# Optimization experiments

Measured on AMD Instinct MI355X. Metric: run time of the kernel, lower is better.

The kernel has to match this reference:

```python
import math
import jax, jax.numpy as jnp
import numpy as np

HEADS = 8
LOG_APPROX_VAR = math.log(0.01)  # self.var = 0.01, non-trainable


def clustering(x, approx_log_var, mu, log_var, log_prior):
    """Faithful port of DisentangledAttention.clustering (mi_estimation=False).
    x: [B,H,L,D]; approx_log_var: [B,H,L]; mu/log_var: [H,C,D]; log_prior: [H,C].
    Returns (cluster_probs [B,H,L,C], kl_loss [B,1,1], div_loss [B])."""
    B, H, L, D = x.shape
    xe = x[:, :, :, None, :]                      # [B,H,L,1,D]
    mue = mu[:, None, :, :]                       # [H,1,C,D]
    alv = approx_log_var[:, :, :, None, None]     # [B,H,L,1,1]
    avar = jnp.exp(alv)
    lv = log_var[:, None, :, :]                   # [H,1,C,D]
    var = jnp.exp(lv)
    logp = jax.nn.log_softmax(log_prior, axis=-1)  # [H,C]

    mse = (xe - mue) ** 2 / var                   # [B,H,L,C,D]
    log_pdf = -0.5 * mse.sum(-1) - D * math.pi - 0.5 * lv.sum(-1)  # [B,H,L,C]
    log_pdf = log_pdf + logp[:, None, :]
    log_probs = jax.nn.log_softmax(log_pdf, axis=-1)
    probs = jnp.exp(log_probs)                    # [B,H,L,C]

    logp_b = logp[None, :, None, :]               # broadcast prior log-probs
    prior = jnp.exp(logp_b)
    # F.kl_div(log_probs, prior) = prior * (log(prior) - log_probs)
    kl = (prior * (logp_b - log_probs)).sum(-1).mean(axis=(1, 2))            # [B]
    kl = kl + 0.5 * (probs * (mse + avar / var + lv).sum(-1)).sum(-1).mean(axis=(1, 2))
    kl = kl - 0.5 * jnp.mean(((1.0 + alv).sum(-1)) * D, axis=(1, 2, 3))
    kl_loss = kl.reshape(-1, 1, 1)

    eyeL = jnp.eye(L, dtype=x.dtype)
    div = jnp.einsum('bhqc,bhkc->bhqk', probs, probs)   # [B,H,L,L]
    div = (div - eyeL) ** 2
    wmask = eyeL * 1.25 + (1.0 - eyeL) * 0.75
    div_loss = (div * wmask).mean(axis=(1, 2, 3))       # [B]
    return probs, kl_loss, div_loss


def setup_inputs() -> dict:
    k = jax.random.key(0)
    ks = jax.random.split(k, 10)
    B, L, D, H, C = 4, 1024, 512, HEADS, 8
    Dk = D // H
    lin_std = 1.0 / math.sqrt(2.0 * D)  # xavier_normal gain=1/sqrt(2)
    return {
        'query': jax.random.normal(ks[0], (B, L, D), jnp.float32),
        'key': jax.random.normal(ks[1], (B, L, D), jnp.float32),
        'value': jax.random.normal(ks[2], (B, L, D), jnp.float32),
        'padding_mask': jnp.zeros((B, 1, L), jnp.float32),
        'Wq': jax.random.normal(ks[3], (D, D), jnp.float32) * lin_std,
        'bq': jnp.zeros((D,), jnp.float32),
        'Wk': jax.random.normal(ks[4], (D, D), jnp.float32) * lin_std,
        'bk': jnp.zeros((D,), jnp.float32),
        'Wv': jax.random.normal(ks[5], (D, D), jnp.float32) * lin_std,
        'bv': jnp.zeros((D,), jnp.float32),
        'Wo': jax.random.normal(ks[6], (D, D), jnp.float32) * lin_std,
        'bo': jnp.zeros((D,), jnp.float32),
        'tok_mu': jax.random.normal(ks[7], (H, C, Dk), jnp.float32) * 0.1,
        'tok_log_var': jnp.zeros((H, C, Dk), jnp.float32),
        'tok_log_prior': jnp.full((H, C), math.log(1.0 / C), jnp.float32),
    }


def reference(query, key, value, padding_mask, Wq, bq, Wk, bk, Wv, bv, Wo, bo,
              tok_mu, tok_log_var, tok_log_prior):
    B, L, D = query.shape
    H = HEADS
    Dk = D // H

    # GMM clustering on raw (unprojected) per-head query/key, eval mode (no reparam noise)
    qh = query.reshape(B, L, H, Dk).transpose(0, 2, 1, 3)  # [B,H,L,Dk]
    kh = key.reshape(B, L, H, Dk).transpose(0, 2, 1, 3)
    alv = jnp.full((B, H, L), LOG_APPROX_VAR, dtype=query.dtype)
    probs_q, kl_q, div_q = clustering(qh, alv, tok_mu, tok_log_var, tok_log_prior)
    probs_k, kl_k, div_k = clustering(kh, alv, tok_mu, tok_log_var, tok_log_prior)

    # Disentangled mask: tokens sharing clusters attend (mask==1 means blocked)
    sim = jnp.einsum('bhqc,bhkc->bhqk', probs_q, probs_k)   # [B,H,L,L]
    cmask = jnp.clip(1.0 - sim + padding_mask[:, :, None, :], 0.0, 1.0)

    # Projections + scaled softmax attention (per softmax_attention/full_attention)
    q = (query @ Wq.T + bq).reshape(B, L, H, Dk).transpose(0, 2, 1, 3) / math.sqrt(Dk)
    kk = (key @ Wk.T + bk).reshape(B, L, H, Dk).transpose(0, 2, 1, 3)
    v = (value @ Wv.T + bv).reshape(B, L, H, Dk).transpose(0, 2, 1, 3)
    scores = jnp.einsum('bhqd,bhkd->bhqk', q, kk) + jax.lax.stop_gradient(cmask) * (-10000.0)
    attn = jax.nn.softmax(scores, axis=-1) * (1.0 - cmask)
    out = jnp.einsum('bhqk,bhkd->bhqd', attn, v).transpose(0, 2, 1, 3).reshape(B, L, D)
    out = out @ Wo.T + bo

    kl_loss = kl_q + kl_k                      # [B,1,1]
    div_loss = (div_q + div_k).reshape(-1, 1, 1)  # [B,1,1]
    return out, kl_loss, div_loss
```

## Files before the change

kernel.cpp:

```cpp
#include <hip/hip_runtime.h>
#include <hip/hip_bf16.h>
#include <math.h>

#define NB 4
#define NL 1024
#define ND 512
#define NH 8
#define NC 8
#define NDK 64

static constexpr float KL3_CONST = 115.36544595161891f;

typedef __bf16 bf16x8 __attribute__((ext_vector_type(8)));
typedef float  f32x4v __attribute__((ext_vector_type(4)));
typedef unsigned short u16x4 __attribute__((ext_vector_type(4)));
typedef unsigned short u16x8 __attribute__((ext_vector_type(8)));

__device__ __forceinline__ unsigned short bf16u(float f) {
    return __builtin_bit_cast(unsigned short, (__bf16)f);
}

struct GemmArgs {
    const void* A; const float* W; const float* bias; void* out;
    float scale; int abf; int obf; int brow; int ostr; int vmap;
};

#define GEMM_BUF 15360

__device__ __forceinline__ void gemm_body(const GemmArgs& g, unsigned char* smem)
{
    const int tid = threadIdx.x;
    int n0, m0;
    if (g.vmap) {
        const int linear = blockIdx.y * 4 + blockIdx.x;
        n0 = (linear & 31) * 128;
        m0 = (linear >> 5) * 64;
    } else {
        n0 = blockIdx.x * 128;
        m0 = blockIdx.y * 64;
    }

    const int w = tid >> 6, lane = tid & 63;
    const int r16 = lane & 15, quad = lane >> 4;
    const int arow = tid >> 2, akc = tid & 3;
    const int wrow = tid >> 1, wkc = tid & 1;

    f32x4v acc[8];
#pragma unroll
    for (int n = 0; n < 8; ++n) acc[n] = (f32x4v){0.f, 0.f, 0.f, 0.f};

    auto ldA = [&](int k0) -> u16x8 {
        if (g.abf) {
            return *(const u16x8*)((const unsigned short*)g.A + (size_t)(m0 + arow) * 512 + k0 + akc * 8);
        }
        const float* ap = (const float*)g.A + (size_t)(m0 + arow) * 512 + k0 + akc * 8;
        const float4 a0 = *(const float4*)ap, a1 = *(const float4*)(ap + 4);
        return (u16x8){ bf16u(a0.x), bf16u(a0.y), bf16u(a0.z), bf16u(a0.w),
                        bf16u(a1.x), bf16u(a1.y), bf16u(a1.z), bf16u(a1.w) };
    };
    auto ldW = [&](int k0, u16x8* dst) {
        const float* wp = (const float*)g.W + (size_t)(n0 + wrow) * 512 + k0 + wkc * 16;
        const float4 w0 = *(const float4*)wp,       w1 = *(const float4*)(wp + 4);
        const float4 w2 = *(const float4*)(wp + 8), w3 = *(const float4*)(wp + 12);
        dst[0] = (u16x8){ bf16u(w0.x), bf16u(w0.y), bf16u(w0.z), bf16u(w0.w),
                          bf16u(w1.x), bf16u(w1.y), bf16u(w1.z), bf16u(w1.w) };
        dst[1] = (u16x8){ bf16u(w2.x), bf16u(w2.y), bf16u(w2.z), bf16u(w2.w),
                          bf16u(w3.x), bf16u(w3.y), bf16u(w3.z), bf16u(w3.w) };
    };
    auto store_stage = [&](int buf, const u16x8& sa, const u16x8* sw) {
        unsigned short* As = (unsigned short*)(smem + buf * GEMM_BUF);
        unsigned short* Ws = (unsigned short*)(smem + buf * GEMM_BUF + 5120);
        *(u16x8*)(As + arow * 40 + akc * 8) = sa;
        *(u16x8*)(Ws + wrow * 40 + wkc * 16) = sw[0];
        *(u16x8*)(Ws + wrow * 40 + wkc * 16 + 8) = sw[1];
    };
    auto mfma_half = [&](int buf) {
        unsigned short* As = (unsigned short*)(smem + buf * GEMM_BUF);
        unsigned short* Ws = (unsigned short*)(smem + buf * GEMM_BUF + 5120);
        bf16x8 af = *(const bf16x8*)(As + (w * 16 + r16) * 40 + quad * 8);
#pragma unroll
        for (int ni = 0; ni < 8; ++ni) {
            bf16x8 bfr = *(const bf16x8*)(Ws + (ni * 16 + r16) * 40 + quad * 8);
            acc[ni] = __builtin_amdgcn_mfma_f32_16x16x32_bf16(af, bfr, acc[ni], 0, 0, 0);
        }
    };

    u16x8 sa0 = ldA(0),  sw0[2]; ldW(0, sw0);
    u16x8 sa1 = ldA(32), sw1[2]; ldW(32, sw1);
    store_stage(0, sa0, sw0);
    sa0 = ldA(64); ldW(64, sw0);

    for (int p = 0; p < 16; p += 2) {
        const int kbase = p * 32;
        __syncthreads();
        store_stage(1, sa1, sw1);
        if (kbase + 96 < 512) { sa1 = ldA(kbase + 96); ldW(kbase + 96, sw1); }
        mfma_half(0);

        __syncthreads();
        if (p + 2 < 16) store_stage(0, sa0, sw0);
        if (kbase + 128 < 512) { sa0 = ldA(kbase + 128); ldW(kbase + 128, sw0); }
        mfma_half(1);
    }

#pragma unroll
    for (int ni = 0; ni < 8; ++ni) {
        const int col = n0 + ni * 16 + r16;
        const float bcol = g.brow ? 0.f : g.bias[col];
#pragma unroll
        for (int i = 0; i < 4; ++i) {
            const int row = m0 + w * 16 + quad * 4 + i;
            const float bv = g.brow ? g.bias[row] : bcol;
            const float v = (acc[ni][i] + bv) * g.scale;
            if (g.obf) ((unsigned short*)g.out)[(size_t)row * g.ostr + col] = bf16u(v);
            else       ((float*)g.out)[(size_t)row * g.ostr + col] = v;
        }
    }
}

#define GEMM_BUF64 10240

__device__ __forceinline__ void gemm_body64(const GemmArgs& g, unsigned char* smem)
{
    const int tid = threadIdx.x;
    const int n0 = blockIdx.x * 64, m0 = blockIdx.y * 64;

    const int w = tid >> 6, lane = tid & 63;
    const int r16 = lane & 15, quad = lane >> 4;
    const int arow = tid >> 2, akc = tid & 3;

    f32x4v acc[4];
#pragma unroll
    for (int n = 0; n < 4; ++n) acc[n] = (f32x4v){0.f, 0.f, 0.f, 0.f};

    auto ldA = [&](int k0) -> u16x8 {
        if (g.abf) {
            return *(const u16x8*)((const unsigned short*)g.A + (size_t)(m0 + arow) * 512 + k0 + akc * 8);
        }
        const float* ap = (const float*)g.A + (size_t)(m0 + arow) * 512 + k0 + akc * 8;
        const float4 a0 = *(const float4*)ap, a1 = *(const float4*)(ap + 4);
        return (u16x8){ bf16u(a0.x), bf16u(a0.y), bf16u(a0.z), bf16u(a0.w),
                        bf16u(a1.x), bf16u(a1.y), bf16u(a1.z), bf16u(a1.w) };
    };
    auto ldW8 = [&](int k0) -> u16x8 {
        const float* wp = (const float*)g.W + (size_t)(n0 + arow) * 512 + k0 + akc * 8;
        const float4 w0 = *(const float4*)wp, w1 = *(const float4*)(wp + 4);
        return (u16x8){ bf16u(w0.x), bf16u(w0.y), bf16u(w0.z), bf16u(w0.w),
                        bf16u(w1.x), bf16u(w1.y), bf16u(w1.z), bf16u(w1.w) };
    };
    auto store_stage = [&](int buf, const u16x8& sa, const u16x8& sw) {
        unsigned short* As = (unsigned short*)(smem + buf * GEMM_BUF64);
        unsigned short* Ws = (unsigned short*)(smem + buf * GEMM_BUF64 + 5120);
        *(u16x8*)(As + arow * 40 + akc * 8) = sa;
        *(u16x8*)(Ws + arow * 40 + akc * 8) = sw;
    };
    auto mfma_half = [&](int buf) {
        unsigned short* As = (unsigned short*)(smem + buf * GEMM_BUF64);
        unsigned short* Ws = (unsigned short*)(smem + buf * GEMM_BUF64 + 5120);
        bf16x8 af = *(const bf16x8*)(As + (w * 16 + r16) * 40 + quad * 8);
#pragma unroll
        for (int ni = 0; ni < 4; ++ni) {
            bf16x8 bfr = *(const bf16x8*)(Ws + (ni * 16 + r16) * 40 + quad * 8);
            acc[ni] = __builtin_amdgcn_mfma_f32_16x16x32_bf16(af, bfr, acc[ni], 0, 0, 0);
        }
    };

    u16x8 sa0 = ldA(0),  sw0 = ldW8(0);
    u16x8 sa1 = ldA(32), sw1 = ldW8(32);
    store_stage(0, sa0, sw0);
    sa0 = ldA(64); sw0 = ldW8(64);

    for (int p = 0; p < 16; p += 2) {
        const int kbase = p * 32;
        __syncthreads();
        store_stage(1, sa1, sw1);
        if (kbase + 96 < 512) { sa1 = ldA(kbase + 96); sw1 = ldW8(kbase + 96); }
        mfma_half(0);

        __syncthreads();
        if (p + 2 < 16) store_stage(0, sa0, sw0);
        if (kbase + 128 < 512) { sa0 = ldA(kbase + 128); sw0 = ldW8(kbase + 128); }
        mfma_half(1);
    }

#pragma unroll
    for (int ni = 0; ni < 4; ++ni) {
        const int col = n0 + ni * 16 + r16;
        const float bcol = g.brow ? 0.f : g.bias[col];
#pragma unroll
        for (int i = 0; i < 4; ++i) {
            const int row = m0 + w * 16 + quad * 4 + i;
            const float bv = g.brow ? g.bias[row] : bcol;
            const float v = (acc[ni][i] + bv) * g.scale;
            if (g.obf) ((unsigned short*)g.out)[(size_t)row * g.ostr + col] = bf16u(v);
            else       ((float*)g.out)[(size_t)row * g.ostr + col] = v;
        }
    }
}

__device__ __forceinline__ void cluster_body(
    const float* __restrict__ query, const float* __restrict__ key,
    const float* __restrict__ tok_mu, const float* __restrict__ tok_log_var,
    const float* __restrict__ tok_log_prior,
    float* __restrict__ probs_q, float* __restrict__ probs_k,
    float* __restrict__ klp, float* __restrict__ divp, float* __restrict__ Gp,
    int linear, unsigned char* smem)
{
    float* mu_s    = (float*)smem;
    float* iv_s    = (float*)(smem + 2048);
    float* Pl      = (float*)(smem + 4096);
    float* Gpart   = (float*)(smem + 13312);
    float* red_s   = (float*)(smem + 14336);
    float* lvsum_s = (float*)(smem + 14368);
    float* alpha_s = (float*)(smem + 14400);
    float* logp_s  = (float*)(smem + 14432);
    float* prior_s = (float*)(smem + 14464);

    const int tid  = threadIdx.x;
    const int side = linear >> 7;
    const int rem  = linear & 127;
    const int bh   = rem >> 2, chunk = rem & 3;
    const int b    = bh >> 3, h = bh & 7;
    const int blocklin = side * 128 + bh * 4 + chunk;
    const float* src = side ? key : query;
    float* probs_out = side ? probs_k : probs_q;

    for (int i = tid; i < 512; i += 256) {
        mu_s[i] = tok_mu[h * 512 + i];
        float lv = tok_log_var[h * 512 + i];
        iv_s[i] = __expf(-lv);
    }
    if (tid < 8) {
        float ls = 0.f, al = 0.f;
        for (int d = 0; d < 64; ++d) {
            float lv = tok_log_var[(h * 8 + tid) * 64 + d];
            ls += lv;
            al += 0.01f * __expf(-lv) + lv;
        }
        lvsum_s[tid] = ls; alpha_s[tid] = al;
    }
    if (tid == 0) {
        float lp[8]; float mx = -1e30f;
        for (int c = 0; c < 8; ++c) { lp[c] = tok_log_prior[h * 8 + c]; mx = fmaxf(mx, lp[c]); }
        float se = 0.f;
        for (int c = 0; c < 8; ++c) se += __expf(lp[c] - mx);
        float lse = mx + __logf(se);
        for (int c = 0; c < 8; ++c) { logp_s[c] = lp[c] - lse; prior_s[c] = __expf(lp[c] - lse); }
    }
    __syncthreads();

    const int l = chunk * 256 + tid;
    const float4* xp = (const float4*)(src + ((size_t)(b * NL + l)) * ND + h * NDK);
    float4 xr[16];
#pragma unroll
    for (int i = 0; i < 16; ++i) xr[i] = xp[i];

    float ms[8];
#pragma unroll
    for (int c = 0; c < 8; ++c) {
        const float4* mc = (const float4*)(mu_s + c * 64);
        const float4* ic = (const float4*)(iv_s + c * 64);
        float s = 0.f;
#pragma unroll
        for (int i = 0; i < 16; ++i) {
            float4 m4 = mc[i], v4 = ic[i], x4 = xr[i];
            float dx = x4.x - m4.x; s = fmaf(dx * dx, v4.x, s);
            float dy = x4.y - m4.y; s = fmaf(dy * dy, v4.y, s);
            float dz = x4.z - m4.z; s = fmaf(dz * dz, v4.z, s);
            float dw = x4.w - m4.w; s = fmaf(dw * dw, v4.w, s);
        }
        ms[c] = s;
    }

    float lpdf[8]; float mx = -1e30f;
#pragma unroll
    for (int c = 0; c < 8; ++c) {
        lpdf[c] = -0.5f * (ms[c] + lvsum_s[c]) + logp_s[c];
        mx = fmaxf(mx, lpdf[c]);
    }
    float e[8]; float se = 0.f;
#pragma unroll
    for (int c = 0; c < 8; ++c) { e[c] = __expf(lpdf[c] - mx); se += e[c]; }
    float lse = __logf(se);
    float inv = 1.f / se;
    float p[8]; float kl1 = 0.f, kl2 = 0.f, sqq = 0.f;
#pragma unroll
    for (int c = 0; c < 8; ++c) {
        p[c] = e[c] * inv;
        float logprob = lpdf[c] - mx - lse;
        kl1 += prior_s[c] * (logp_s[c] - logprob);
        kl2 += p[c] * (ms[c] + alpha_s[c]);
        sqq = fmaf(p[c], p[c], sqq);
    }

    float* po = probs_out + ((size_t)((b * NH + h) * NL + l)) * NC;
    ((float4*)po)[0] = make_float4(p[0], p[1], p[2], p[3]);
    ((float4*)po)[1] = make_float4(p[4], p[5], p[6], p[7]);
#pragma unroll
    for (int c = 0; c < 8; ++c) Pl[tid * 9 + c] = p[c];

    float dterm = 1.25f * (sqq - 1.f) * (sqq - 1.f) - 0.75f * sqq * sqq;
    float klv = kl1 + 0.5f * kl2;
    __syncthreads();

    {
        int qt = tid >> 6, pos = tid & 63, c1 = pos >> 3, c2 = pos & 7;
        float g = 0.f;
        for (int i = 0; i < 64; ++i) {
            int ll = qt * 64 + i;
            g = fmaf(Pl[ll * 9 + c1], Pl[ll * 9 + c2], g);
        }
        Gpart[qt * 64 + pos] = g;
    }

#pragma unroll
    for (int o = 32; o > 0; o >>= 1) {
        klv   += __shfl_down(klv, o);
        dterm += __shfl_down(dterm, o);
    }
    if ((tid & 63) == 0) { red_s[tid >> 6] = klv; red_s[4 + (tid >> 6)] = dterm; }
    __syncthreads();
    if (tid == 0) {
        klp[blocklin]  = red_s[0] + red_s[1] + red_s[2] + red_s[3];
        divp[blocklin] = red_s[4] + red_s[5] + red_s[6] + red_s[7];
    }
    if (tid < 64)
        Gp[(size_t)blocklin * 64 + tid] =
            Gpart[tid] + Gpart[64 + tid] + Gpart[128 + tid] + Gpart[192 + tid];
}

__global__ __launch_bounds__(256) void fused_front(
    GemmArgs g0, GemmArgs g1, GemmArgs g2,
    const float* query, const float* key,
    const float* tok_mu, const float* tok_log_var, const float* tok_log_prior,
    float* probs_q, float* probs_k,
    float* klp, float* divp, float* Gp)
{
    __shared__ alignas(16) unsigned char smem[2 * GEMM_BUF];
    if (blockIdx.z == 3) {
        const int linear = blockIdx.y * 4 + blockIdx.x;
        cluster_body(query, key, tok_mu, tok_log_var, tok_log_prior,
                     probs_q, probs_k, klp, divp, Gp, linear, smem);
        return;
    }
    GemmArgs g = (blockIdx.z == 0) ? g0 : ((blockIdx.z == 1) ? g1 : g2);
    gemm_body(g, smem);
}

#define APAD 72

__global__ __launch_bounds__(256) void attn_mfma6_kernel(
    const unsigned short* __restrict__ qp16, const unsigned short* __restrict__ kp16,
    const unsigned short* __restrict__ vtp16,
    const float* __restrict__ probs_q, const float* __restrict__ probs_k,
    const float* __restrict__ padding_mask,
    float* __restrict__ pO, float* __restrict__ pML)
{
    const int tid = threadIdx.x, lane = tid & 63, w = tid >> 6;
    const int r16 = lane & 15, quad = lane >> 4;
    const int b = blockIdx.z >> 1, s = blockIdx.z & 1;
    const int h = blockIdx.y;
    const int qt = blockIdx.x;
    const int qbase = qt * 64;

    __shared__ alignas(16) unsigned short Ks[2][64 * APAD];
    __shared__ alignas(16) unsigned short Vt[2][64 * APAD];
    __shared__ alignas(16) unsigned short Ps[4][16 * APAD];
    __shared__ float pk_s[2][8 * 65];
    __shared__ float pm_s[2][64];

    const int c0row = tid >> 3,        c0c8 = tid & 7;
    const int c1row = (tid + 256) >> 3, c1c8 = tid & 7;
    const int pkey = tid >> 1, phalf = tid & 1;

    bf16x8 qa[2];
    {
        const unsigned short* qrow = qp16 + ((size_t)(b * NL + qbase + w * 16 + r16)) * ND + h * NDK;
        qa[0] = *(const bf16x8*)(qrow + quad * 8);
        qa[1] = *(const bf16x8*)(qrow + 32 + quad * 8);
    }
    float pq[4][8];
#pragma unroll
    for (int i = 0; i < 4; ++i) {
        const float* pr = probs_q + ((size_t)((b * NH + h) * NL + qbase + w * 16 + quad * 4 + i)) * NC;
        float4 a = ((const float4*)pr)[0], c = ((const float4*)pr)[1];
        pq[i][0] = a.x; pq[i][1] = a.y; pq[i][2] = a.z; pq[i][3] = a.w;
        pq[i][4] = c.x; pq[i][5] = c.y; pq[i][6] = c.z; pq[i][7] = c.w;
    }

    f32x4v oacc[4];
#pragma unroll
    for (int n = 0; n < 4; ++n) oacc[n] = (f32x4v){0.f, 0.f, 0.f, 0.f};
    float m_i[4] = {-1e30f, -1e30f, -1e30f, -1e30f};
    float l_i[4] = {0.f, 0.f, 0.f, 0.f};

    u16x8 rk0, rk1, rv0, rv1;
    float4 rpk;
    float rpm;

    auto stage_load = [&](int kt) {
        const int key0 = s * 512 + kt * 64;
        rk0 = *(const u16x8*)(kp16 + ((size_t)(b * NL + key0 + c0row)) * ND + h * NDK + c0c8 * 8);
        rk1 = *(const u16x8*)(kp16 + ((size_t)(b * NL + key0 + c1row)) * ND + h * NDK + c1c8 * 8);
        rv0 = *(const u16x8*)(vtp16 + ((size_t)(h * 64 + c0row)) * (NB * NL) + b * NL + key0 + c0c8 * 8);
        rv1 = *(const u16x8*)(vtp16 + ((size_t)(h * 64 + c1row)) * (NB * NL) + b * NL + key0 + c1c8 * 8);
        if (tid < 128)
            rpk = *(const float4*)(probs_k + ((size_t)((b * NH + h) * NL + key0 + pkey)) * NC + phalf * 4);
        if (tid < 64)
            rpm = padding_mask[b * NL + key0 + tid];
    };
    auto stage_store = [&](int buf) {
        *(u16x8*)(Ks[buf] + c0row * APAD + c0c8 * 8) = rk0;
        *(u16x8*)(Ks[buf] + c1row * APAD + c1c8 * 8) = rk1;
        *(u16x8*)(Vt[buf] + c0row * APAD + c0c8 * 8) = rv0;
        *(u16x8*)(Vt[buf] + c1row * APAD + c1c8 * 8) = rv1;
        if (tid < 128) {
            pk_s[buf][(phalf * 4 + 0) * 65 + pkey] = rpk.x;
            pk_s[buf][(phalf * 4 + 1) * 65 + pkey] = rpk.y;
            pk_s[buf][(phalf * 4 + 2) * 65 + pkey] = rpk.z;
            pk_s[buf][(phalf * 4 + 3) * 65 + pkey] = rpk.w;
        }
        if (tid < 64) pm_s[buf][tid] = rpm;
    };

    stage_load(0);
    stage_store(0);
    stage_load(1);

    for (int kt = 0; kt < 8; ++kt) {
        const int cur = kt & 1;
        __syncthreads();

        f32x4v sacc[4];
#pragma unroll
        for (int t = 0; t < 4; ++t) {
            sacc[t] = (f32x4v){0.f, 0.f, 0.f, 0.f};
            bf16x8 kb0 = *(const bf16x8*)(Ks[cur] + (t * 16 + r16) * APAD + quad * 8);
            bf16x8 kb1 = *(const bf16x8*)(Ks[cur] + (t * 16 + r16) * APAD + 32 + quad * 8);
            sacc[t] = __builtin_amdgcn_mfma_f32_16x16x32_bf16(qa[0], kb0, sacc[t], 0, 0, 0);
            sacc[t] = __builtin_amdgcn_mfma_f32_16x16x32_bf16(qa[1], kb1, sacc[t], 0, 0, 0);
        }

        float sc[4][4], wgt[4][4];
#pragma unroll
        for (int t = 0; t < 4; ++t) {
            const int keyl = t * 16 + r16;
            float pkc[8];
#pragma unroll
            for (int c = 0; c < 8; ++c) pkc[c] = pk_s[cur][c * 65 + keyl];
            const float pmv = pm_s[cur][keyl];
#pragma unroll
            for (int i = 0; i < 4; ++i) {
                float sim = 0.f;
#pragma unroll
                for (int c = 0; c < 8; ++c) sim = fmaf(pq[i][c], pkc[c], sim);
                float cm = 1.f - sim + pmv;
                cm = fminf(fmaxf(cm, 0.f), 1.f);
                sc[t][i] = sacc[t][i] - 10000.f * cm;
                wgt[t][i] = 1.f - cm;
            }
        }

        float mx[4];
#pragma unroll
        for (int i = 0; i < 4; ++i)
            mx[i] = fmaxf(fmaxf(sc[0][i], sc[1][i]), fmaxf(sc[2][i], sc[3][i]));
#pragma unroll
        for (int o = 1; o < 16; o <<= 1) {
#pragma unroll
            for (int i = 0; i < 4; ++i) mx[i] = fmaxf(mx[i], __shfl_xor(mx[i], o));
        }
        float rr[4];
#pragma unroll
        for (int i = 0; i < 4; ++i) {
            const float mnew = fmaxf(m_i[i], mx[i]);
            rr[i] = __expf(m_i[i] - mnew);
            m_i[i] = mnew;
            l_i[i] *= rr[i];
        }
#pragma unroll
        for (int n = 0; n < 4; ++n) {
            oacc[n][0] *= rr[0]; oacc[n][1] *= rr[1];
            oacc[n][2] *= rr[2]; oacc[n][3] *= rr[3];
        }
        float lad[4] = {0.f, 0.f, 0.f, 0.f};
#pragma unroll
        for (int t = 0; t < 4; ++t) {
#pragma unroll
            for (int i = 0; i < 4; ++i) {
                const float p = __expf(sc[t][i] - m_i[i]);
                lad[i] += p;
                Ps[w][(quad * 4 + i) * APAD + t * 16 + r16] = bf16u(p * wgt[t][i]);
            }
        }
#pragma unroll
        for (int o = 1; o < 16; o <<= 1) {
#pragma unroll
            for (int i = 0; i < 4; ++i) lad[i] += __shfl_xor(lad[i], o);
        }
#pragma unroll
        for (int i = 0; i < 4; ++i) l_i[i] += lad[i];

        bf16x8 pa0 = *(const bf16x8*)(Ps[w] + r16 * APAD + quad * 8);
        bf16x8 pa1 = *(const bf16x8*)(Ps[w] + r16 * APAD + 32 + quad * 8);
#pragma unroll
        for (int n = 0; n < 4; ++n) {
            bf16x8 vb0 = *(const bf16x8*)(Vt[cur] + (n * 16 + r16) * APAD + quad * 8);
            bf16x8 vb1 = *(const bf16x8*)(Vt[cur] + (n * 16 + r16) * APAD + 32 + quad * 8);
            oacc[n] = __builtin_amdgcn_mfma_f32_16x16x32_bf16(pa0, vb0, oacc[n], 0, 0, 0);
            oacc[n] = __builtin_amdgcn_mfma_f32_16x16x32_bf16(pa1, vb1, oacc[n], 0, 0, 0);
        }

        if (kt < 7) stage_store(cur ^ 1);
        if (kt < 6) stage_load(kt + 2);
    }

    const int sb32 = (((b * 8 + h) << 5) | (qt * 2 + (w >> 1)));
    float* po = pO + ((size_t)sb32 * 2 + s) * 2048;
#pragma unroll
    for (int i = 0; i < 4; ++i) {
        const int row = (w & 1) * 16 + quad * 4 + i;
#pragma unroll
        for (int n = 0; n < 4; ++n)
            po[row * 64 + n * 16 + r16] = oacc[n][i];
    }
    if (r16 == 0) {
        float* pml = pML + ((size_t)sb32 * 2 + s) * 64;
#pragma unroll
        for (int i = 0; i < 4; ++i) {
            const int row = (w & 1) * 16 + quad * 4 + i;
            pml[row * 2]     = m_i[i];
            pml[row * 2 + 1] = l_i[i];
        }
    }
}

__device__ __forceinline__ void finalize_body(
    const float* __restrict__ klp, const float* __restrict__ divp,
    const float* __restrict__ Gp, float* __restrict__ out_tail)
{
    const int tid = threadIdx.x, b = tid >> 6, lane = tid & 63;
    float gsum = 0.f;
#pragma unroll
    for (int s = 0; s < 2; ++s)
#pragma unroll
        for (int h = 0; h < 8; ++h) {
            const int base = s * 128 + (b * 8 + h) * 4;
            float Ge = 0.f;
#pragma unroll
            for (int x = 0; x < 4; ++x) Ge += Gp[(size_t)(base + x) * 64 + lane];
            gsum = fmaf(Ge, Ge, gsum);
        }
    const int s = lane >> 5, rem = lane & 31, h = rem >> 2, x = rem & 3;
    const int idx = s * 128 + (b * 8 + h) * 4 + x;
    float klv = klp[idx];
    float dvv = divp[idx];
#pragma unroll
    for (int o = 32; o > 0; o >>= 1) {
        gsum += __shfl_down(gsum, o);
        klv  += __shfl_down(klv, o);
        dvv  += __shfl_down(dvv, o);
    }
    if (lane == 0) {
        out_tail[b]     = klv * (1.0f / 8192.0f) + 2.0f * KL3_CONST;
        out_tail[4 + b] = (dvv + 0.75f * gsum) * (1.0f / 8388608.0f);
    }
}

__global__ __launch_bounds__(256) void merge_fin_kernel(
    const float* __restrict__ pO, const float* __restrict__ pML,
    unsigned short* __restrict__ ao16,
    const float* __restrict__ klp, const float* __restrict__ divp,
    const float* __restrict__ Gp, float* __restrict__ out_tail)
{
    if (blockIdx.x == 1024) { finalize_body(klp, divp, Gp, out_tail); return; }
    const int gid = blockIdx.x * 256 + threadIdx.x;
    const int sb = gid >> 8, rem = gid & 255;
    const int row = rem >> 3, d0 = (rem & 7) * 8;

    const float2 ml0 = *(const float2*)(pML + ((size_t)sb * 2 + 0) * 64 + row * 2);
    const float2 ml1 = *(const float2*)(pML + ((size_t)sb * 2 + 1) * 64 + row * 2);
    const float M = fmaxf(ml0.x, ml1.x);
    const float e0 = __expf(ml0.x - M), e1 = __expf(ml1.x - M);
    const float inv = 1.f / fmaf(ml0.y, e0, ml1.y * e1);
    const float f0 = e0 * inv, f1 = e1 * inv;

    const float* p0 = pO + ((size_t)sb * 2 + 0) * 2048 + row * 64 + d0;
    const float* p1 = pO + ((size_t)sb * 2 + 1) * 2048 + row * 64 + d0;
    const int qt = sb & 31, bh = sb >> 5, h = bh & 7, b = bh >> 3;
    unsigned short* orow = ao16 + ((size_t)(b * NL + qt * 32 + row)) * ND + h * NDK + d0;

    const float4 a0 = *(const float4*)p0,       a1 = *(const float4*)(p0 + 4);
    const float4 c0 = *(const float4*)p1,       c1 = *(const float4*)(p1 + 4);
    u16x8 ov = { bf16u(a0.x * f0 + c0.x * f1), bf16u(a0.y * f0 + c0.y * f1),
                 bf16u(a0.z * f0 + c0.z * f1), bf16u(a0.w * f0 + c0.w * f1),
                 bf16u(a1.x * f0 + c1.x * f1), bf16u(a1.y * f0 + c1.y * f1),
                 bf16u(a1.z * f0 + c1.z * f1), bf16u(a1.w * f0 + c1.w * f1) };
    *(u16x8*)orow = ov;
}

__global__ __launch_bounds__(256) void gemm_single64(GemmArgs g)
{
    __shared__ alignas(16) unsigned char smem[2 * GEMM_BUF64];
    gemm_body64(g, smem);
}

extern "C" void kernel_launch(void* const* d_in, const int* in_sizes, int n_in,
                              void* d_out, int out_size, void* d_ws, size_t ws_size,
                              hipStream_t stream)
{
    const float* query        = (const float*)d_in[0];
    const float* key          = (const float*)d_in[1];
    const float* value        = (const float*)d_in[2];
    const float* padding_mask = (const float*)d_in[3];
    const float* Wq = (const float*)d_in[4];
    const float* bq = (const float*)d_in[5];
    const float* Wk = (const float*)d_in[6];
    const float* bk = (const float*)d_in[7];
    const float* Wv = (const float*)d_in[8];
    const float* bv = (const float*)d_in[9];
    const float* Wo = (const float*)d_in[10];
    const float* bo = (const float*)d_in[11];
    const float* tok_mu        = (const float*)d_in[12];
    const float* tok_log_var   = (const float*)d_in[13];
    const float* tok_log_prior = (const float*)d_in[14];

    float* ws = (float*)d_ws;
    const size_t FS = 1048576;
    unsigned short* qp16  = (unsigned short*)ws;
    unsigned short* kp16  = (unsigned short*)(ws + FS);
    unsigned short* vtp16 = (unsigned short*)(ws + 2 * FS);
    unsigned short* ao16  = (unsigned short*)(ws + 3 * FS);
    float* probs_q = ws + 4 * FS;
    float* probs_k = probs_q + (size_t)NB * NH * NL * NC;
    float* pO      = probs_k + (size_t)NB * NH * NL * NC;
    float* pML     = pO + 4194304;
    float* klp     = pML + 131072;
    float* divp    = klp + 256;
    float* Gp      = divp + 256;

    GemmArgs gq {query, Wq, bq, qp16, 0.125f, 0, 1, 0, 512, 0};
    GemmArgs gk {key,   Wk, bk, kp16, 1.f,    0, 1, 0, 512, 0};
    GemmArgs gvt{Wv, value, bv, vtp16, 1.f,   0, 1, 1, 4096, 1};
    fused_front<<<dim3(4, 64, 4), 256, 0, stream>>>(
        gq, gk, gvt, query, key, tok_mu, tok_log_var, tok_log_prior,
        probs_q, probs_k, klp, divp, Gp);

    attn_mfma6_kernel<<<dim3(16, NH, NB * 2), 256, 0, stream>>>(
        qp16, kp16, vtp16, probs_q, probs_k, padding_mask, pO, pML);

    merge_fin_kernel<<<1025, 256, 0, stream>>>(
        pO, pML, ao16, klp, divp, Gp, (float*)d_out + (size_t)NB * NL * ND);

    GemmArgs go{ao16, Wo, bo, d_out, 1.f, 1, 0, 0, 512, 0};
    gemm_single64<<<dim3(8, 64, 1), 256, 0, stream>>>(go);
}
```

Baseline: 190.7 us.

## Drop split-KV attention and merge kernel; normalize output directly in attention

Attention no longer splits the key range into two halves. Each block now walks all 1024 keys and writes the normalized bf16 output straight to ao16. This removes the separate merge kernel, its launch, and the fp32 partial O/ML round trip through global memory. The finalize reduction moves into an extra block column of the attention grid. The cost is half as many attention blocks (512 instead of 1024) and a serial loop twice as long, which lowers parallelism on a GPU with many CUs.

```diff
diff --git a/kernel.cpp b/kernel.cpp
--- a/kernel.cpp
+++ b/kernel.cpp
@@ -347,18 +347,57 @@
     gemm_body(g, smem);
 }
 
+__device__ __forceinline__ void finalize_body(
+    const float* __restrict__ klp, const float* __restrict__ divp,
+    const float* __restrict__ Gp, float* __restrict__ out_tail)
+{
+    const int tid = threadIdx.x, b = tid >> 6, lane = tid & 63;
+    float gsum = 0.f;
+#pragma unroll
+    for (int s = 0; s < 2; ++s)
+#pragma unroll
+        for (int h = 0; h < 8; ++h) {
+            const int base = s * 128 + (b * 8 + h) * 4;
+            float Ge = 0.f;
+#pragma unroll
+            for (int x = 0; x < 4; ++x) Ge += Gp[(size_t)(base + x) * 64 + lane];
+            gsum = fmaf(Ge, Ge, gsum);
+        }
+    const int s = lane >> 5, rem = lane & 31, h = rem >> 2, x = rem & 3;
+    const int idx = s * 128 + (b * 8 + h) * 4 + x;
+    float klv = klp[idx];
+    float dvv = divp[idx];
+#pragma unroll
+    for (int o = 32; o > 0; o >>= 1) {
+        gsum += __shfl_down(gsum, o);
+        klv  += __shfl_down(klv, o);
+        dvv  += __shfl_down(dvv, o);
+    }
+    if (lane == 0) {
+        out_tail[b]     = klv * (1.0f / 8192.0f) + 2.0f * KL3_CONST;
+        out_tail[4 + b] = (dvv + 0.75f * gsum) * (1.0f / 8388608.0f);
+    }
+}
+
 #define APAD 72
 
-__global__ __launch_bounds__(256) void attn_mfma6_kernel(
+__global__ __launch_bounds__(256) void attn_mfma7_kernel(
     const unsigned short* __restrict__ qp16, const unsigned short* __restrict__ kp16,
     const unsigned short* __restrict__ vtp16,
     const float* __restrict__ probs_q, const float* __restrict__ probs_k,
     const float* __restrict__ padding_mask,
-    float* __restrict__ pO, float* __restrict__ pML)
-{
+    unsigned short* __restrict__ ao16,
+    const float* __restrict__ klp, const float* __restrict__ divp,
+    const float* __restrict__ Gp, float* __restrict__ out_tail)
+{
+    if (blockIdx.x == 16) {
+        if (blockIdx.y == 0 && blockIdx.z == 0) finalize_body(klp, divp, Gp, out_tail);
+        return;
+    }
+
     const int tid = threadIdx.x, lane = tid & 63, w = tid >> 6;
     const int r16 = lane & 15, quad = lane >> 4;
-    const int b = blockIdx.z >> 1, s = blockIdx.z & 1;
+    const int b = blockIdx.z;
     const int h = blockIdx.y;
     const int qt = blockIdx.x;
     const int qbase = qt * 64;
@@ -399,7 +438,7 @@
     float rpm;
 
     auto stage_load = [&](int kt) {
-        const int key0 = s * 512 + kt * 64;
+        const int key0 = kt * 64;
         rk0 = *(const u16x8*)(kp16 + ((size_t)(b * NL + key0 + c0row)) * ND + h * NDK + c0c8 * 8);
         rk1 = *(const u16x8*)(kp16 + ((size_t)(b * NL + key0 + c1row)) * ND + h * NDK + c1c8 * 8);
         rv0 = *(const u16x8*)(vtp16 + ((size_t)(h * 64 + c0row)) * (NB * NL) + b * NL + key0 + c0c8 * 8);
@@ -427,7 +466,7 @@
     stage_store(0);
     stage_load(1);
 
-    for (int kt = 0; kt < 8; ++kt) {
+    for (int kt = 0; kt < 16; ++kt) {
         const int cur = kt & 1;
         __syncthreads();
 
@@ -511,92 +550,18 @@
             oacc[n] = __builtin_amdgcn_mfma_f32_16x16x32_bf16(pa1, vb1, oacc[n], 0, 0, 0);
         }
 
-        if (kt < 7) stage_store(cur ^ 1);
-        if (kt < 6) stage_load(kt + 2);
-    }
-
-    const int sb32 = (((b * 8 + h) << 5) | (qt * 2 + (w >> 1)));
-    float* po = pO + ((size_t)sb32 * 2 + s) * 2048;
+        if (kt < 15) stage_store(cur ^ 1);
+        if (kt < 14) stage_load(kt + 2);
+    }
+
 #pragma unroll
     for (int i = 0; i < 4; ++i) {
-        const int row = (w & 1) * 16 + quad * 4 + i;
+        const float invl = 1.f / l_i[i];
+        unsigned short* orow = ao16 + ((size_t)(b * NL + qbase + w * 16 + quad * 4 + i)) * ND + h * NDK;
 #pragma unroll
         for (int n = 0; n < 4; ++n)
-            po[row * 64 + n * 16 + r16] = oacc[n][i];
-    }
-    if (r16 == 0) {
-        float* pml = pML + ((size_t)sb32 * 2 + s) * 64;
-#pragma unroll
-        for (int i = 0; i < 4; ++i) {
-            const int row = (w & 1) * 16 + quad * 4 + i;
-            pml[row * 2]     = m_i[i];
-            pml[row * 2 + 1] = l_i[i];
-        }
-    }
-}
-
-__device__ __forceinline__ void finalize_body(
-    const float* __restrict__ klp, const float* __restrict__ divp,
-    const float* __restrict__ Gp, float* __restrict__ out_tail)
-{
-    const int tid = threadIdx.x, b = tid >> 6, lane = tid & 63;
-    float gsum = 0.f;
-#pragma unroll
-    for (int s = 0; s < 2; ++s)
-#pragma unroll
-        for (int h = 0; h < 8; ++h) {
-            const int base = s * 128 + (b * 8 + h) * 4;
-            float Ge = 0.f;
-#pragma unroll
-            for (int x = 0; x < 4; ++x) Ge += Gp[(size_t)(base + x) * 64 + lane];
-            gsum = fmaf(Ge, Ge, gsum);
-        }
-    const int s = lane >> 5, rem = lane & 31, h = rem >> 2, x = rem & 3;
-    const int idx = s * 128 + (b * 8 + h) * 4 + x;
-    float klv = klp[idx];
-    float dvv = divp[idx];
-#pragma unroll
-    for (int o = 32; o > 0; o >>= 1) {
-        gsum += __shfl_down(gsum, o);
-        klv  += __shfl_down(klv, o);
-        dvv  += __shfl_down(dvv, o);
-    }
-    if (lane == 0) {
-        out_tail[b]     = klv * (1.0f / 8192.0f) + 2.0f * KL3_CONST;
-        out_tail[4 + b] = (dvv + 0.75f * gsum) * (1.0f / 8388608.0f);
-    }
-}
-
-__global__ __launch_bounds__(256) void merge_fin_kernel(
-    const float* __restrict__ pO, const float* __restrict__ pML,
-    unsigned short* __restrict__ ao16,
-    const float* __restrict__ klp, const float* __restrict__ divp,
-    const float* __restrict__ Gp, float* __restrict__ out_tail)
-{
-    if (blockIdx.x == 1024) { finalize_body(klp, divp, Gp, out_tail); return; }
-    const int gid = blockIdx.x * 256 + threadIdx.x;
-    const int sb = gid >> 8, rem = gid & 255;
-    const int row = rem >> 3, d0 = (rem & 7) * 8;
-
-    const float2 ml0 = *(const float2*)(pML + ((size_t)sb * 2 + 0) * 64 + row * 2);
-    const float2 ml1 = *(const float2*)(pML + ((size_t)sb * 2 + 1) * 64 + row * 2);
-    const float M = fmaxf(ml0.x, ml1.x);
-    const float e0 = __expf(ml0.x - M), e1 = __expf(ml1.x - M);
-    const float inv = 1.f / fmaf(ml0.y, e0, ml1.y * e1);
-    const float f0 = e0 * inv, f1 = e1 * inv;
-
-    const float* p0 = pO + ((size_t)sb * 2 + 0) * 2048 + row * 64 + d0;
-    const float* p1 = pO + ((size_t)sb * 2 + 1) * 2048 + row * 64 + d0;
-    const int qt = sb & 31, bh = sb >> 5, h = bh & 7, b = bh >> 3;
-    unsigned short* orow = ao16 + ((size_t)(b * NL + qt * 32 + row)) * ND + h * NDK + d0;
-
-    const float4 a0 = *(const float4*)p0,       a1 = *(const float4*)(p0 + 4);
-    const float4 c0 = *(const float4*)p1,       c1 = *(const float4*)(p1 + 4);
-    u16x8 ov = { bf16u(a0.x * f0 + c0.x * f1), bf16u(a0.y * f0 + c0.y * f1),
-                 bf16u(a0.z * f0 + c0.z * f1), bf16u(a0.w * f0 + c0.w * f1),
-                 bf16u(a1.x * f0 + c1.x * f1), bf16u(a1.y * f0 + c1.y * f1),
-                 bf16u(a1.z * f0 + c1.z * f1), bf16u(a1.w * f0 + c1.w * f1) };
-    *(u16x8*)orow = ov;
+            orow[n * 16 + r16] = bf16u(oacc[n][i] * invl);
+    }
 }
 
 __global__ __launch_bounds__(256) void gemm_single64(GemmArgs g)
@@ -633,9 +598,7 @@
     unsigned short* ao16  = (unsigned short*)(ws + 3 * FS);
     float* probs_q = ws + 4 * FS;
     float* probs_k = probs_q + (size_t)NB * NH * NL * NC;
-    float* pO      = probs_k + (size_t)NB * NH * NL * NC;
-    float* pML     = pO + 4194304;
-    float* klp     = pML + 131072;
+    float* klp     = probs_k + (size_t)NB * NH * NL * NC;
     float* divp    = klp + 256;
     float* Gp      = divp + 256;
 
@@ -646,11 +609,9 @@
         gq, gk, gvt, query, key, tok_mu, tok_log_var, tok_log_prior,
         probs_q, probs_k, klp, divp, Gp);
 
-    attn_mfma6_kernel<<<dim3(16, NH, NB * 2), 256, 0, stream>>>(
-        qp16, kp16, vtp16, probs_q, probs_k, padding_mask, pO, pML);
-
-    merge_fin_kernel<<<1025, 256, 0, stream>>>(
-        pO, pML, ao16, klp, divp, Gp, (float*)d_out + (size_t)NB * NL * ND);
+    attn_mfma7_kernel<<<dim3(17, NH, NB), 256, 0, stream>>>(
+        qp16, kp16, vtp16, probs_q, probs_k, padding_mask, ao16,
+        klp, divp, Gp, (float*)d_out + (size_t)NB * NL * ND);
 
     GemmArgs go{ao16, Wo, bo, d_out, 1.f, 1, 0, 0, 512, 0};
     gemm_single64<<<dim3(8, 64, 1), 256, 0, stream>>>(go);
```

Result: slower. 205.1 us (+7.5%).

## Fuse split-KV merge into attention kernel via last-arriver atomic counter

Applied to the files above, without the earlier changes.

Drops the separate merge kernel. Each pair of split-KV attention blocks now increments a per-tile atomic counter, and the second block to arrive combines both partial outputs into the bf16 attention buffer. The finalize reduction moves into an extra grid column of the attention kernel. This saves one kernel launch and its tail. In exchange it adds a memset launch, threadfences and an atomic per block, and the merge work is serialized onto the late-arriving blocks.

```diff
diff --git a/kernel.cpp b/kernel.cpp
--- a/kernel.cpp
+++ b/kernel.cpp
@@ -347,15 +347,56 @@
     gemm_body(g, smem);
 }
 
+__device__ __forceinline__ void finalize_body(
+    const float* __restrict__ klp, const float* __restrict__ divp,
+    const float* __restrict__ Gp, float* __restrict__ out_tail)
+{
+    const int tid = threadIdx.x, b = tid >> 6, lane = tid & 63;
+    float gsum = 0.f;
+#pragma unroll
+    for (int s = 0; s < 2; ++s)
+#pragma unroll
+        for (int h = 0; h < 8; ++h) {
+            const int base = s * 128 + (b * 8 + h) * 4;
+            float Ge = 0.f;
+#pragma unroll
+            for (int x = 0; x < 4; ++x) Ge += Gp[(size_t)(base + x) * 64 + lane];
+            gsum = fmaf(Ge, Ge, gsum);
+        }
+    const int s = lane >> 5, rem = lane & 31, h = rem >> 2, x = rem & 3;
+    const int idx = s * 128 + (b * 8 + h) * 4 + x;
+    float klv = klp[idx];
+    float dvv = divp[idx];
+#pragma unroll
+    for (int o = 32; o > 0; o >>= 1) {
+        gsum += __shfl_down(gsum, o);
+        klv  += __shfl_down(klv, o);
+        dvv  += __shfl_down(dvv, o);
+    }
+    if (lane == 0) {
+        out_tail[b]     = klv * (1.0f / 8192.0f) + 2.0f * KL3_CONST;
+        out_tail[4 + b] = (dvv + 0.75f * gsum) * (1.0f / 8388608.0f);
+    }
+}
+
 #define APAD 72
 
-__global__ __launch_bounds__(256) void attn_mfma6_kernel(
+__global__ __launch_bounds__(256) void attn_mfma8_kernel(
     const unsigned short* __restrict__ qp16, const unsigned short* __restrict__ kp16,
     const unsigned short* __restrict__ vtp16,
     const float* __restrict__ probs_q, const float* __restrict__ probs_k,
     const float* __restrict__ padding_mask,
-    float* __restrict__ pO, float* __restrict__ pML)
-{
+    float* __restrict__ pO, float* __restrict__ pML,
+    unsigned short* __restrict__ ao16, unsigned int* __restrict__ cnt,
+    const float* __restrict__ klp, const float* __restrict__ divp,
+    const float* __restrict__ Gp, float* __restrict__ out_tail)
+{
+    if (blockIdx.x == 16) {
+        if (blockIdx.y == 0 && blockIdx.z == 0)
+            finalize_body(klp, divp, Gp, out_tail);
+        return;
+    }
+
     const int tid = threadIdx.x, lane = tid & 63, w = tid >> 6;
     const int r16 = lane & 15, quad = lane >> 4;
     const int b = blockIdx.z >> 1, s = blockIdx.z & 1;
@@ -368,6 +409,7 @@
     __shared__ alignas(16) unsigned short Ps[4][16 * APAD];
     __shared__ float pk_s[2][8 * 65];
     __shared__ float pm_s[2][64];
+    __shared__ unsigned int old_s;
 
     const int c0row = tid >> 3,        c0c8 = tid & 7;
     const int c1row = (tid + 256) >> 3, c1c8 = tid & 7;
@@ -533,70 +575,38 @@
             pml[row * 2 + 1] = l_i[i];
         }
     }
-}
-
-__device__ __forceinline__ void finalize_body(
-    const float* __restrict__ klp, const float* __restrict__ divp,
-    const float* __restrict__ Gp, float* __restrict__ out_tail)
-{
-    const int tid = threadIdx.x, b = tid >> 6, lane = tid & 63;
-    float gsum = 0.f;
-#pragma unroll
-    for (int s = 0; s < 2; ++s)
-#pragma unroll
-        for (int h = 0; h < 8; ++h) {
-            const int base = s * 128 + (b * 8 + h) * 4;
-            float Ge = 0.f;
-#pragma unroll
-            for (int x = 0; x < 4; ++x) Ge += Gp[(size_t)(base + x) * 64 + lane];
-            gsum = fmaf(Ge, Ge, gsum);
-        }
-    const int s = lane >> 5, rem = lane & 31, h = rem >> 2, x = rem & 3;
-    const int idx = s * 128 + (b * 8 + h) * 4 + x;
-    float klv = klp[idx];
-    float dvv = divp[idx];
-#pragma unroll
-    for (int o = 32; o > 0; o >>= 1) {
-        gsum += __shfl_down(gsum, o);
-        klv  += __shfl_down(klv, o);
-        dvv  += __shfl_down(dvv, o);
-    }
-    if (lane == 0) {
-        out_tail[b]     = klv * (1.0f / 8192.0f) + 2.0f * KL3_CONST;
-        out_tail[4 + b] = (dvv + 0.75f * gsum) * (1.0f / 8388608.0f);
-    }
-}
-
-__global__ __launch_bounds__(256) void merge_fin_kernel(
-    const float* __restrict__ pO, const float* __restrict__ pML,
-    unsigned short* __restrict__ ao16,
-    const float* __restrict__ klp, const float* __restrict__ divp,
-    const float* __restrict__ Gp, float* __restrict__ out_tail)
-{
-    if (blockIdx.x == 1024) { finalize_body(klp, divp, Gp, out_tail); return; }
-    const int gid = blockIdx.x * 256 + threadIdx.x;
-    const int sb = gid >> 8, rem = gid & 255;
-    const int row = rem >> 3, d0 = (rem & 7) * 8;
-
-    const float2 ml0 = *(const float2*)(pML + ((size_t)sb * 2 + 0) * 64 + row * 2);
-    const float2 ml1 = *(const float2*)(pML + ((size_t)sb * 2 + 1) * 64 + row * 2);
-    const float M = fmaxf(ml0.x, ml1.x);
-    const float e0 = __expf(ml0.x - M), e1 = __expf(ml1.x - M);
-    const float inv = 1.f / fmaf(ml0.y, e0, ml1.y * e1);
-    const float f0 = e0 * inv, f1 = e1 * inv;
-
-    const float* p0 = pO + ((size_t)sb * 2 + 0) * 2048 + row * 64 + d0;
-    const float* p1 = pO + ((size_t)sb * 2 + 1) * 2048 + row * 64 + d0;
-    const int qt = sb & 31, bh = sb >> 5, h = bh & 7, b = bh >> 3;
-    unsigned short* orow = ao16 + ((size_t)(b * NL + qt * 32 + row)) * ND + h * NDK + d0;
-
-    const float4 a0 = *(const float4*)p0,       a1 = *(const float4*)(p0 + 4);
-    const float4 c0 = *(const float4*)p1,       c1 = *(const float4*)(p1 + 4);
-    u16x8 ov = { bf16u(a0.x * f0 + c0.x * f1), bf16u(a0.y * f0 + c0.y * f1),
-                 bf16u(a0.z * f0 + c0.z * f1), bf16u(a0.w * f0 + c0.w * f1),
-                 bf16u(a1.x * f0 + c1.x * f1), bf16u(a1.y * f0 + c1.y * f1),
-                 bf16u(a1.z * f0 + c1.z * f1), bf16u(a1.w * f0 + c1.w * f1) };
-    *(u16x8*)orow = ov;
+
+    __threadfence();
+    __syncthreads();
+    if (tid == 0) old_s = atomicAdd(&cnt[(b * NH + h) * 16 + qt], 1u);
+    __syncthreads();
+    if (old_s == 0u) return;
+    __threadfence();
+
+    {
+        const int r = tid >> 2, cseg = (tid & 3) * 16;
+        const int sbm = (((b * 8 + h) << 5) | (qt * 2 + (r >> 5)));
+        const int rrow = r & 31;
+        const float2 ml0 = *(const float2*)(pML + ((size_t)sbm * 2 + 0) * 64 + rrow * 2);
+        const float2 ml1 = *(const float2*)(pML + ((size_t)sbm * 2 + 1) * 64 + rrow * 2);
+        const float M = fmaxf(ml0.x, ml1.x);
+        const float e0 = __expf(ml0.x - M), e1 = __expf(ml1.x - M);
+        const float inv = 1.f / fmaf(ml0.y, e0, ml1.y * e1);
+        const float f0 = e0 * inv, f1 = e1 * inv;
+        const float* p0 = pO + ((size_t)sbm * 2 + 0) * 2048 + rrow * 64 + cseg;
+        const float* p1 = pO + ((size_t)sbm * 2 + 1) * 2048 + rrow * 64 + cseg;
+        unsigned short* orow = ao16 + ((size_t)(b * NL + qt * 64 + r)) * ND + h * NDK + cseg;
+#pragma unroll
+        for (int u = 0; u < 2; ++u) {
+            const float4 a0 = *(const float4*)(p0 + u * 8), a1 = *(const float4*)(p0 + u * 8 + 4);
+            const float4 c0 = *(const float4*)(p1 + u * 8), c1 = *(const float4*)(p1 + u * 8 + 4);
+            u16x8 ov = { bf16u(a0.x * f0 + c0.x * f1), bf16u(a0.y * f0 + c0.y * f1),
+                         bf16u(a0.z * f0 + c0.z * f1), bf16u(a0.w * f0 + c0.w * f1),
+                         bf16u(a1.x * f0 + c1.x * f1), bf16u(a1.y * f0 + c1.y * f1),
+                         bf16u(a1.z * f0 + c1.z * f1), bf16u(a1.w * f0 + c1.w * f1) };
+            *(u16x8*)(orow + u * 8) = ov;
+        }
+    }
 }
 
 __global__ __launch_bounds__(256) void gemm_single64(GemmArgs g)
@@ -638,6 +648,9 @@
     float* klp     = pML + 131072;
     float* divp    = klp + 256;
     float* Gp      = divp + 256;
+    unsigned int* cnt = (unsigned int*)(Gp + 16384);
+
+    hipMemsetAsync(cnt, 0, 512 * sizeof(unsigned int), stream);
 
     GemmArgs gq {query, Wq, bq, qp16, 0.125f, 0, 1, 0, 512, 0};
     GemmArgs gk {key,   Wk, bk, kp16, 1.f,    0, 1, 0, 512, 0};
@@ -646,11 +659,9 @@
         gq, gk, gvt, query, key, tok_mu, tok_log_var, tok_log_prior,
         probs_q, probs_k, klp, divp, Gp);
 
-    attn_mfma6_kernel<<<dim3(16, NH, NB * 2), 256, 0, stream>>>(
-        qp16, kp16, vtp16, probs_q, probs_k, padding_mask, pO, pML);
-
-    merge_fin_kernel<<<1025, 256, 0, stream>>>(
-        pO, pML, ao16, klp, divp, Gp, (float*)d_out + (size_t)NB * NL * ND);
+    attn_mfma8_kernel<<<dim3(17, NH, NB * 2), 256, 0, stream>>>(
+        qp16, kp16, vtp16, probs_q, probs_k, padding_mask, pO, pML,
+        ao16, cnt, klp, divp, Gp, (float*)d_out + (size_t)NB * NL * ND);
 
     GemmArgs go{ao16, Wo, bo, d_out, 1.f, 1, 0, 0, 512, 0};
     gemm_single64<<<dim3(8, 64, 1), 256, 0, stream>>>(go);
```

Result: slower. 363.2 us (+90.4%).
